# Kernel tuning notes

Measured on AMD Instinct MI355X. Metric: run time of the kernel, lower is better.

## Reference

```python
import jax, jax.numpy as jnp
import numpy as np

D_MODEL = 1024
N_HEADS = 16
HEAD_DIM = D_MODEL // N_HEADS
D_FF = 4096
B, T = 2, 2048


def layernorm(x, g, b, eps=1e-5):
    mu = jnp.mean(x, axis=-1, keepdims=True)
    var = jnp.var(x, axis=-1, keepdims=True)
    return (x - mu) * jax.lax.rsqrt(var + eps) * g + b


def setup_inputs() -> dict:
    key = jax.random.key(0)
    ks = jax.random.split(key, 8)
    s = 0.02
    return {
        "x": jax.random.normal(ks[0], (B, T, D_MODEL), dtype=jnp.float32),
        "ln1_g": jnp.ones((D_MODEL,), jnp.float32),
        "ln1_b": jnp.zeros((D_MODEL,), jnp.float32),
        "qkv_w": jax.random.normal(ks[1], (D_MODEL, 3 * D_MODEL), jnp.float32) * s,
        "qkv_b": jnp.zeros((3 * D_MODEL,), jnp.float32),
        "proj_w": jax.random.normal(ks[2], (D_MODEL, D_MODEL), jnp.float32) * s,
        "proj_b": jnp.zeros((D_MODEL,), jnp.float32),
        "ln2_g": jnp.ones((D_MODEL,), jnp.float32),
        "ln2_b": jnp.zeros((D_MODEL,), jnp.float32),
        "mlp_w1": jax.random.normal(ks[3], (D_MODEL, D_FF), jnp.float32) * s,
        "mlp_b1": jnp.zeros((D_FF,), jnp.float32),
        "mlp_w2": jax.random.normal(ks[4], (D_FF, D_MODEL), jnp.float32) * s,
        "mlp_b2": jnp.zeros((D_MODEL,), jnp.float32),
    }


def reference(x, ln1_g, ln1_b, qkv_w, qkv_b, proj_w, proj_b,
              ln2_g, ln2_b, mlp_w1, mlp_b1, mlp_w2, mlp_b2):
    Bv, Tv, C = x.shape
    scale = HEAD_DIM ** -0.5
    # --- attention branch ---
    h = layernorm(x, ln1_g, ln1_b)
    qkv = h @ qkv_w + qkv_b                                   # [B,T,3C]
    qkv = qkv.reshape(Bv, Tv, 3, N_HEADS, HEAD_DIM)
    q, k, v = qkv[:, :, 0], qkv[:, :, 1], qkv[:, :, 2]        # [B,T,H,Dh]
    att = jnp.einsum('bqhd,bkhd->bhqk', q, k) * scale         # [B,H,T,T]
    causal = jnp.tril(jnp.ones((Tv, Tv), dtype=bool))
    att = jnp.where(causal[None, None], att, -jnp.inf)
    att = jax.nn.softmax(att, axis=-1)
    out = jnp.einsum('bhqk,bkhd->bqhd', att, v).reshape(Bv, Tv, C)
    out = out @ proj_w + proj_b
    x = x + out
    # --- mlp branch ---
    h2 = layernorm(x, ln2_g, ln2_b)
    h2 = jax.nn.gelu(h2 @ mlp_w1 + mlp_b1, approximate=False)
    x = x + (h2 @ mlp_w2 + mlp_b2)
    return x
```

## Files before the change

### kernel.cpp

```cpp
#include <hip/hip_runtime.h>
#include <hip/hip_bf16.h>
#include <cstdint>

typedef __attribute__((ext_vector_type(4))) float f32x4;
typedef __attribute__((ext_vector_type(16))) float f32x16;
typedef __attribute__((ext_vector_type(8))) __bf16 bf16x8;
typedef __attribute__((ext_vector_type(4))) __bf16 bf16x4;
typedef __attribute__((ext_vector_type(4))) uint32_t u32x4;
typedef __attribute__((ext_vector_type(2))) unsigned int u32x2;

#define EPI_BF16  0
#define EPI_GELU  1
#define EPI_RES   2
#define EPI_PART  3
#define EPI_PARTB 4

__device__ __forceinline__ void gll16(const void* g, void* l) {
  __builtin_amdgcn_global_load_lds((__attribute__((address_space(1))) void*)(g),
                                   (__attribute__((address_space(3))) void*)(l), 16, 0, 0);
}

__global__ __launch_bounds__(256)
void convT_all(const float* __restrict__ W0, __bf16* __restrict__ T0,
               const float* __restrict__ W1, __bf16* __restrict__ T1,
               const float* __restrict__ W2, __bf16* __restrict__ T2,
               const float* __restrict__ W3, __bf16* __restrict__ T3)
{
  __shared__ __bf16 t[64][72];
  const int bid = blockIdx.x;
  const float* W; __bf16* WT; int Kd, Nd, nx, lb;
  if (bid < 768)       { W = W0; WT = T0; Kd = 1024; Nd = 3072; nx = 48; lb = bid; }
  else if (bid < 1024) { W = W1; WT = T1; Kd = 1024; Nd = 1024; nx = 16; lb = bid - 768; }
  else if (bid < 2048) { W = W2; WT = T2; Kd = 1024; Nd = 4096; nx = 64; lb = bid - 1024; }
  else                 { W = W3; WT = T3; Kd = 4096; Nd = 1024; nx = 16; lb = bid - 2048; }
  const int tid = threadIdx.x;
  const int n0 = (lb % nx) * 64, k0 = (lb / nx) * 64;
#pragma unroll
  for (int i = 0; i < 4; ++i) {
    const int c = i * 256 + tid;
    const int r = c >> 4, cc = (c & 15) * 4;
    const float4 v = *(const float4*)(W + (size_t)(k0 + r) * Nd + n0 + cc);
    bf16x4 tv; tv[0] = (__bf16)v.x; tv[1] = (__bf16)v.y; tv[2] = (__bf16)v.z; tv[3] = (__bf16)v.w;
    *(bf16x4*)&t[r][cc] = tv;
  }
  __syncthreads();
#pragma unroll
  for (int i = 0; i < 2; ++i) {
    const int c = i * 256 + tid;
    const int n = c >> 3, s = (c & 7) * 8;
    bf16x8 o;
#pragma unroll
    for (int j = 0; j < 8; ++j) o[j] = t[s + j][n];
    *(bf16x8*)(WT + (size_t)(n0 + n) * Kd + k0 + s) = o;
  }
}

__global__ __launch_bounds__(256)
void ln_rows(const float* __restrict__ x, const float* __restrict__ g,
             const float* __restrict__ b, __bf16* __restrict__ out)
{
  const int row = blockIdx.x;
  const int tid = threadIdx.x;
  const float4 v = *(const float4*)(x + (size_t)row * 1024 + tid * 4);
  float s = v.x + v.y + v.z + v.w;
  float q = v.x * v.x + v.y * v.y + v.z * v.z + v.w * v.w;
#pragma unroll
  for (int o = 32; o; o >>= 1) { s += __shfl_xor(s, o); q += __shfl_xor(q, o); }
  __shared__ float red[8];
  const int wid = tid >> 6;
  if ((tid & 63) == 0) { red[wid] = s; red[4 + wid] = q; }
  __syncthreads();
  s = red[0] + red[1] + red[2] + red[3];
  q = red[4] + red[5] + red[6] + red[7];
  const float mu = s * (1.0f / 1024.0f);
  const float var = q * (1.0f / 1024.0f) - mu * mu;
  const float rs = rsqrtf(var + 1e-5f);
  bf16x4 o4;
#pragma unroll
  for (int i = 0; i < 4; ++i) {
    const int c = tid * 4 + i;
    const float xv = (&v.x)[i];
    o4[i] = (__bf16)((xv - mu) * rs * g[c] + b[c]);
  }
  *(bf16x4*)(out + (size_t)row * 1024 + tid * 4) = o4;
}

template<int EPI>
__global__ __launch_bounds__(256)
void gemm_bt(const __bf16* __restrict__ A, const __bf16* __restrict__ BT,
             const float* __restrict__ bias, const float* __restrict__ R,
             void* __restrict__ Out, int M, int N, int K)
{
  const int tid = threadIdx.x;
  const int lane = tid & 63, wid = tid >> 6;
  const int l15 = lane & 15, lg = lane >> 4;
  const int wm = (wid >> 1) * 64, wn = (wid & 1) * 64;
  const int nwg = gridDim.x * gridDim.y;
  const int hw = blockIdx.y * gridDim.x + blockIdx.x;
  const int logical = (hw & 7) * (nwg >> 3) + (hw >> 3);
  const int rowBase = (logical / gridDim.x) * 128;
  const int colBase = (logical % gridDim.x) * 128;
  const int kLen = K / gridDim.z;
  const int kBeg = blockIdx.z * kLen;
  __shared__ __bf16 As[2][128 * 32];
  __shared__ __bf16 Bs[2][128 * 32];
  f32x4 acc[4][4] = {};
  const int fsw = ((l15 >> 1) & 3) << 3;

  auto STAGE = [&](int buf, int k0) {
#pragma unroll
    for (int i = 0; i < 2; ++i) {
      const int c = i * 256 + tid;
      const int r = c >> 2;
      const int s = ((c & 3) ^ ((r >> 1) & 3)) * 8;
      gll16(A + (size_t)(rowBase + r) * K + (k0 + s), &As[buf][c * 8]);
      gll16(BT + (size_t)(colBase + r) * K + (k0 + s), &Bs[buf][c * 8]);
    }
  };

  STAGE(0, kBeg);
  __syncthreads();
  int cur = 0;
  const int kEnd = kBeg + kLen;
  for (int k0 = kBeg; k0 < kEnd; k0 += 32) {
    if (k0 + 32 < kEnd) STAGE(cur ^ 1, k0 + 32);
    bf16x8 af[4], bfr[4];
#pragma unroll
    for (int m = 0; m < 4; ++m) af[m] = *(const bf16x8*)(&As[cur][(wm + m * 16 + l15) * 32 + (lg * 8 ^ fsw)]);
#pragma unroll
    for (int n = 0; n < 4; ++n) bfr[n] = *(const bf16x8*)(&Bs[cur][(wn + n * 16 + l15) * 32 + (lg * 8 ^ fsw)]);
#pragma unroll
    for (int m = 0; m < 4; ++m)
#pragma unroll
      for (int n = 0; n < 4; ++n)
        acc[m][n] = __builtin_amdgcn_mfma_f32_16x16x32_bf16(af[m], bfr[n], acc[m][n], 0, 0, 0);
    __syncthreads();
    cur ^= 1;
  }
#pragma unroll
  for (int m = 0; m < 4; ++m) {
#pragma unroll
    for (int n = 0; n < 4; ++n) {
      const int col = colBase + wn + n * 16 + l15;
      float bb = 0.0f;
      if constexpr (EPI != EPI_PART && EPI != EPI_PARTB) bb = bias[col];
#pragma unroll
      for (int i = 0; i < 4; ++i) {
        const int row = rowBase + wm + m * 16 + lg * 4 + i;
        float v = acc[m][n][i] + bb;
        if constexpr (EPI == EPI_GELU) {
          v = 0.5f * v * (1.0f + erff(v * 0.70710678118654752f));
          ((__bf16*)Out)[(size_t)row * N + col] = (__bf16)v;
        } else if constexpr (EPI == EPI_BF16) {
          ((__bf16*)Out)[(size_t)row * N + col] = (__bf16)v;
        } else if constexpr (EPI == EPI_RES) {
          v += R[(size_t)row * N + col];
          ((float*)Out)[(size_t)row * N + col] = v;
        } else if constexpr (EPI == EPI_PART) {
          ((float*)Out)[((size_t)blockIdx.z * M + row) * N + col] = v;
        } else {
          ((__bf16*)Out)[((size_t)blockIdx.z * M + row) * N + col] = (__bf16)v;
        }
      }
    }
  }
}

__global__ __launch_bounds__(256)
void reduce2(const float* __restrict__ P, const float* __restrict__ bias,
             const float* __restrict__ R, float* __restrict__ Out, int MN, int N)
{
  const size_t e = ((size_t)blockIdx.x * 256 + threadIdx.x) * 4;
  const float4 a = *(const float4*)(P + e);
  const float4 b = *(const float4*)(P + (size_t)MN + e);
  const float4 r = *(const float4*)(R + e);
  const float4 bb = *(const float4*)(bias + (e & (size_t)(N - 1)));
  float4 o;
  o.x = a.x + b.x + r.x + bb.x;
  o.y = a.y + b.y + r.y + bb.y;
  o.z = a.z + b.z + r.z + bb.z;
  o.w = a.w + b.w + r.w + bb.w;
  *(float4*)(Out + e) = o;
}

__global__ __launch_bounds__(256)
void reduce4(const __bf16* __restrict__ P, const float* __restrict__ bias,
             const float* __restrict__ R, float* __restrict__ Out, int MN, int N)
{
  const size_t e = ((size_t)blockIdx.x * 256 + threadIdx.x) * 8;
  float s[8];
#pragma unroll
  for (int i = 0; i < 8; ++i) s[i] = 0.0f;
#pragma unroll
  for (int p = 0; p < 4; ++p) {
    const bf16x8 v = *(const bf16x8*)(P + (size_t)p * MN + e);
#pragma unroll
    for (int i = 0; i < 8; ++i) s[i] += (float)v[i];
  }
  const size_t col = e & (size_t)(N - 1);
  const float4 r0 = *(const float4*)(R + e),       r1 = *(const float4*)(R + e + 4);
  const float4 b0 = *(const float4*)(bias + col),  b1 = *(const float4*)(bias + col + 4);
  float4 o0, o1;
  o0.x = s[0] + r0.x + b0.x; o0.y = s[1] + r0.y + b0.y;
  o0.z = s[2] + r0.z + b0.z; o0.w = s[3] + r0.w + b0.w;
  o1.x = s[4] + r1.x + b1.x; o1.y = s[5] + r1.y + b1.y;
  o1.z = s[6] + r1.z + b1.z; o1.w = s[7] + r1.w + b1.w;
  *(float4*)(Out + e)     = o0;
  *(float4*)(Out + e + 4) = o1;
}

__global__ __launch_bounds__(256)
void rearrange(const __bf16* __restrict__ qkv, __bf16* __restrict__ Q,
               __bf16* __restrict__ Kb, __bf16* __restrict__ VT)
{
  __shared__ __bf16 vt[64][72];
  const int tid = threadIdx.x;
  const int bid = blockIdx.x;
  const int bh = bid >> 5, tt = bid & 31;
  const int b = bh >> 4, h = bh & 15;
  const int t0 = tt * 64;
#pragma unroll
  for (int i = 0; i < 2; ++i) {
    const int c = i * 256 + tid;
    const int tk = c >> 3, d0 = (c & 7) * 8;
    const size_t srow = (size_t)(b * 2048 + t0 + tk) * 3072 + h * 64 + d0;
    const size_t drow = (size_t)(bh * 2048 + t0 + tk) * 64 + d0;
    *(bf16x8*)(Q + drow) = *(const bf16x8*)(qkv + srow);
    *(bf16x8*)(Kb + drow) = *(const bf16x8*)(qkv + srow + 1024);
    *(bf16x8*)&vt[tk][d0] = *(const bf16x8*)(qkv + srow + 2048);
  }
  __syncthreads();
#pragma unroll
  for (int i = 0; i < 2; ++i) {
    const int c = i * 256 + tid;
    const int d = c >> 3, s = (c & 7) * 8;
    bf16x8 o;
#pragma unroll
    for (int j = 0; j < 8; ++j) o[j] = vt[s + j][d];
    *(bf16x8*)(VT + (size_t)(bh * 64 + d) * 2048 + t0 + s) = o;
  }
}

__global__ __launch_bounds__(256)
void attn(const __bf16* __restrict__ Q, const __bf16* __restrict__ K,
          const __bf16* __restrict__ VT, __bf16* __restrict__ O)
{
  const int bid = blockIdx.x;
  const int bh = bid >> 4, qt = 15 - (bid & 15);
  const int tid = threadIdx.x;
  const int lane = tid & 63, w = tid >> 6;
  const int l31 = lane & 31, hi = lane >> 5;
  __shared__ __bf16 Ks[2][64 * 64];
  __shared__ __bf16 Vs[2][64 * 64];
  const size_t base = (size_t)bh * 2048 * 64;
  const int qrow0 = qt * 128 + w * 32;
  const int jd = qrow0 >> 6;
  const int jmax = 2 * qt + 1;
  const int xsw = (l31 & 7) << 3;
  const float KS = 0.18033688011112042f;

  bf16x8 qf[4];
#pragma unroll
  for (int s = 0; s < 4; ++s)
    qf[s] = *(const bf16x8*)(Q + base + (size_t)(qrow0 + l31) * 64 + s * 16 + hi * 8);

  f32x16 oa0 = {}, oa1 = {};
  float ms = -INFINITY, lst = 0.0f;

  auto STAGE = [&](int buf, int j) {
#pragma unroll
    for (int i = 0; i < 2; ++i) {
      const int c = i * 256 + tid;
      const int r = c >> 3;
      const int e = ((c & 7) ^ (r & 7)) * 8;
      gll16(K + base + (size_t)(j * 64 + r) * 64 + e, &Ks[buf][c * 8]);
      gll16(VT + base + (size_t)r * 2048 + j * 64 + e, &Vs[buf][c * 8]);
    }
  };

  STAGE(0, 0);
  __syncthreads();
  int cur = 0;
  for (int j = 0; j <= jmax; ++j) {
    if (j < jmax) STAGE(cur ^ 1, j + 1);
    if (j <= jd) {
      f32x16 s0v = {}, s1v = {};
#pragma unroll
      for (int s = 0; s < 4; ++s) {
        const int co = (s * 16 + hi * 8) ^ xsw;
        bf16x8 ak0 = *(const bf16x8*)(&Ks[cur][l31 * 64 + co]);
        bf16x8 ak1 = *(const bf16x8*)(&Ks[cur][(32 + l31) * 64 + co]);
        s0v = __builtin_amdgcn_mfma_f32_32x32x16_bf16(ak0, qf[s], s0v, 0, 0, 0);
        s1v = __builtin_amdgcn_mfma_f32_32x32x16_bf16(ak1, qf[s], s1v, 0, 0, 0);
      }
      if (j == jd) {
        const int qg = qrow0 + l31;
#pragma unroll
        for (int rg = 0; rg < 16; ++rg) {
          const int kr = j * 64 + ((rg & 3) + 8 * (rg >> 2)) + 4 * hi;
          if (kr > qg) s0v[rg] = -INFINITY;
          if (kr + 32 > qg) s1v[rg] = -INFINITY;
        }
      }
      float mx = fmaxf(s0v[0], s1v[0]);
#pragma unroll
      for (int rg = 1; rg < 16; ++rg) mx = fmaxf(mx, fmaxf(s0v[rg], s1v[rg]));
      mx = fmaxf(mx, __shfl_xor(mx, 32));
      const float mxs = mx * KS;
      if (!__all(mxs - ms <= 8.0f)) {
        const float msn = fmaxf(ms, mxs);
        const float cf = exp2f(ms - msn);
        lst *= cf;
        ms = msn;
#pragma unroll
        for (int rg = 0; rg < 16; ++rg) {
          const float cb = __shfl(cf, (rg & 3) + 8 * (rg >> 2) + 4 * hi);
          oa0[rg] *= cb; oa1[rg] *= cb;
        }
      }
      float rs = 0.0f;
#pragma unroll
      for (int rg = 0; rg < 16; ++rg) {
        const float p0 = exp2f(fmaf(s0v[rg], KS, -ms));
        const float p1 = exp2f(fmaf(s1v[rg], KS, -ms));
        s0v[rg] = p0; s1v[rg] = p1;
        rs += p0 + p1;
      }
      rs += __shfl_xor(rs, 32);
      lst += rs;
#pragma unroll
      for (int s = 0; s < 4; ++s) {
        const int br = (s & 1) * 8;
        uint32_t wA0, wA1, wB0, wB1;
        if (s < 2) {
          asm("v_cvt_pk_bf16_f32 %0, %1, %2" : "=v"(wA0) : "v"(s0v[br + 0]), "v"(s0v[br + 1]));
          asm("v_cvt_pk_bf16_f32 %0, %1, %2" : "=v"(wA1) : "v"(s0v[br + 2]), "v"(s0v[br + 3]));
          asm("v_cvt_pk_bf16_f32 %0, %1, %2" : "=v"(wB0) : "v"(s0v[br + 4]), "v"(s0v[br + 5]));
          asm("v_cvt_pk_bf16_f32 %0, %1, %2" : "=v"(wB1) : "v"(s0v[br + 6]), "v"(s0v[br + 7]));
        } else {
          asm("v_cvt_pk_bf16_f32 %0, %1, %2" : "=v"(wA0) : "v"(s1v[br + 0]), "v"(s1v[br + 1]));
          asm("v_cvt_pk_bf16_f32 %0, %1, %2" : "=v"(wA1) : "v"(s1v[br + 2]), "v"(s1v[br + 3]));
          asm("v_cvt_pk_bf16_f32 %0, %1, %2" : "=v"(wB0) : "v"(s1v[br + 4]), "v"(s1v[br + 5]));
          asm("v_cvt_pk_bf16_f32 %0, %1, %2" : "=v"(wB1) : "v"(s1v[br + 6]), "v"(s1v[br + 7]));
        }
        const u32x2 r0 = __builtin_amdgcn_permlane32_swap(wA0, wB0, false, false);
        const u32x2 r1 = __builtin_amdgcn_permlane32_swap(wA1, wB1, false, false);
        u32x4 uu; uu.x = r0.x; uu.y = r1.x; uu.z = r0.y; uu.w = r1.y;
        const bf16x8 pa = __builtin_bit_cast(bf16x8, uu);
        const int co = (s * 16 + hi * 8) ^ xsw;
        bf16x8 bv0 = *(const bf16x8*)(&Vs[cur][l31 * 64 + co]);
        bf16x8 bv1 = *(const bf16x8*)(&Vs[cur][(32 + l31) * 64 + co]);
        oa0 = __builtin_amdgcn_mfma_f32_32x32x16_bf16(pa, bv0, oa0, 0, 0, 0);
        oa1 = __builtin_amdgcn_mfma_f32_32x32x16_bf16(pa, bv1, oa1, 0, 0, 0);
      }
    }
    __syncthreads();
    cur ^= 1;
  }
  const float inv = 1.0f / lst;
  const int b = bh >> 4, hd = bh & 15;
#pragma unroll
  for (int rg = 0; rg < 16; ++rg) {
    const int cr = (rg & 3) + 8 * (rg >> 2) + 4 * hi;
    const float ib = __shfl(inv, cr);
    const int qr = qrow0 + cr;
    O[(size_t)(b * 2048 + qr) * 1024 + hd * 64 + l31]      = (__bf16)(oa0[rg] * ib);
    O[(size_t)(b * 2048 + qr) * 1024 + hd * 64 + 32 + l31] = (__bf16)(oa1[rg] * ib);
  }
}

extern "C" void kernel_launch(void* const* d_in, const int* in_sizes, int n_in,
                              void* d_out, int out_size, void* d_ws, size_t ws_size,
                              hipStream_t stream)
{
  const float* x      = (const float*)d_in[0];
  const float* ln1_g  = (const float*)d_in[1];
  const float* ln1_b  = (const float*)d_in[2];
  const float* qkv_w  = (const float*)d_in[3];
  const float* qkv_b  = (const float*)d_in[4];
  const float* proj_w = (const float*)d_in[5];
  const float* proj_b = (const float*)d_in[6];
  const float* ln2_g  = (const float*)d_in[7];
  const float* ln2_b  = (const float*)d_in[8];
  const float* mlp_w1 = (const float*)d_in[9];
  const float* mlp_b1 = (const float*)d_in[10];
  const float* mlp_w2 = (const float*)d_in[11];
  const float* mlp_b2 = (const float*)d_in[12];

  char* ws = (char*)d_ws;
  __bf16* qkvT  = (__bf16*)(ws + 0);
  __bf16* projT = (__bf16*)(ws + 6291456);
  __bf16* w1T   = (__bf16*)(ws + 8388608);
  __bf16* w2T   = (__bf16*)(ws + 16777216);
  float*  x2    = (float*) (ws + 25165824);
  __bf16* h1    = (__bf16*)(ws + 41943040);
  float*  partP = (float*) (ws + 41943040);
  __bf16* part2 = (__bf16*)(ws + 41943040);
  __bf16* qkv   = (__bf16*)(ws + 50331648);
  __bf16* Qb    = (__bf16*)(ws + 75497472);
  __bf16* h2    = (__bf16*)(ws + 75497472);
  __bf16* Kb    = (__bf16*)(ws + 83886080);
  __bf16* act1  = (__bf16*)(ws + 83886080);
  __bf16* VTb   = (__bf16*)(ws + 92274688);
  __bf16* attO  = (__bf16*)(ws + 100663296);

  convT_all<<<3072, 256, 0, stream>>>(qkv_w, qkvT, proj_w, projT, mlp_w1, w1T, mlp_w2, w2T);

  ln_rows<<<4096, 256, 0, stream>>>(x, ln1_g, ln1_b, h1);
  gemm_bt<EPI_BF16><<<dim3(24, 32), 256, 0, stream>>>(h1, qkvT, qkv_b, nullptr, qkv, 4096, 3072, 1024);
  rearrange<<<1024, 256, 0, stream>>>(qkv, Qb, Kb, VTb);
  attn<<<512, 256, 0, stream>>>(Qb, Kb, VTb, attO);
  gemm_bt<EPI_PART><<<dim3(8, 32, 2), 256, 0, stream>>>(attO, projT, nullptr, nullptr, partP, 4096, 1024, 1024);
  reduce2<<<4096, 256, 0, stream>>>(partP, proj_b, x, x2, 4096 * 1024, 1024);
  ln_rows<<<4096, 256, 0, stream>>>(x2, ln2_g, ln2_b, h2);
  gemm_bt<EPI_GELU><<<dim3(32, 32), 256, 0, stream>>>(h2, w1T, mlp_b1, nullptr, act1, 4096, 4096, 1024);
  gemm_bt<EPI_PARTB><<<dim3(8, 32, 4), 256, 0, stream>>>(act1, w2T, nullptr, nullptr, part2, 4096, 1024, 4096);
  reduce4<<<2048, 256, 0, stream>>>(part2, mlp_b2, x2, (float*)d_out, 4096 * 1024, 1024);
}
```

Before: 409.3 us.

## Fuse residual reduce with LayerNorm2 and restructure attention to direct-global loads

```diff
diff --git a/kernel.cpp b/kernel.cpp
--- a/kernel.cpp
+++ b/kernel.cpp
@@ -83,6 +83,47 @@
     o4[i] = (__bf16)((xv - mu) * rs * g[c] + b[c]);
   }
   *(bf16x4*)(out + (size_t)row * 1024 + tid * 4) = o4;
+}
+
+__global__ __launch_bounds__(256)
+void reduce2_ln(const float* __restrict__ P, const float* __restrict__ bias,
+                const float* __restrict__ R, const float* __restrict__ g,
+                const float* __restrict__ b, float* __restrict__ x2,
+                __bf16* __restrict__ h2, int MN)
+{
+  const int row = blockIdx.x;
+  const int tid = threadIdx.x;
+  const size_t e = (size_t)row * 1024 + tid * 4;
+  const float4 a  = *(const float4*)(P + e);
+  const float4 p2 = *(const float4*)(P + (size_t)MN + e);
+  const float4 r  = *(const float4*)(R + e);
+  const float4 bi = *(const float4*)(bias + tid * 4);
+  float v[4];
+  v[0] = a.x + p2.x + r.x + bi.x;
+  v[1] = a.y + p2.y + r.y + bi.y;
+  v[2] = a.z + p2.z + r.z + bi.z;
+  v[3] = a.w + p2.w + r.w + bi.w;
+  *(float4*)(x2 + e) = *(float4*)v;
+  float s = v[0] + v[1] + v[2] + v[3];
+  float q = v[0]*v[0] + v[1]*v[1] + v[2]*v[2] + v[3]*v[3];
+#pragma unroll
+  for (int o = 32; o; o >>= 1) { s += __shfl_xor(s, o); q += __shfl_xor(q, o); }
+  __shared__ float red[8];
+  const int wid = tid >> 6;
+  if ((tid & 63) == 0) { red[wid] = s; red[4 + wid] = q; }
+  __syncthreads();
+  s = red[0] + red[1] + red[2] + red[3];
+  q = red[4] + red[5] + red[6] + red[7];
+  const float mu = s * (1.0f / 1024.0f);
+  const float var = q * (1.0f / 1024.0f) - mu * mu;
+  const float rs = rsqrtf(var + 1e-5f);
+  bf16x4 o4;
+#pragma unroll
+  for (int i = 0; i < 4; ++i) {
+    const int c = tid * 4 + i;
+    o4[i] = (__bf16)((v[i] - mu) * rs * g[c] + b[c]);
+  }
+  *(bf16x4*)(h2 + e) = o4;
 }
 
 template<int EPI>
@@ -167,23 +208,6 @@
 }
 
 __global__ __launch_bounds__(256)
-void reduce2(const float* __restrict__ P, const float* __restrict__ bias,
-             const float* __restrict__ R, float* __restrict__ Out, int MN, int N)
-{
-  const size_t e = ((size_t)blockIdx.x * 256 + threadIdx.x) * 4;
-  const float4 a = *(const float4*)(P + e);
-  const float4 b = *(const float4*)(P + (size_t)MN + e);
-  const float4 r = *(const float4*)(R + e);
-  const float4 bb = *(const float4*)(bias + (e & (size_t)(N - 1)));
-  float4 o;
-  o.x = a.x + b.x + r.x + bb.x;
-  o.y = a.y + b.y + r.y + bb.y;
-  o.z = a.z + b.z + r.z + bb.z;
-  o.w = a.w + b.w + r.w + bb.w;
-  *(float4*)(Out + e) = o;
-}
-
-__global__ __launch_bounds__(256)
 void reduce4(const __bf16* __restrict__ P, const float* __restrict__ bias,
              const float* __restrict__ R, float* __restrict__ Out, int MN, int N)
 {
@@ -241,22 +265,17 @@
   }
 }
 
-__global__ __launch_bounds__(256)
+__global__ __launch_bounds__(128)
 void attn(const __bf16* __restrict__ Q, const __bf16* __restrict__ K,
           const __bf16* __restrict__ VT, __bf16* __restrict__ O)
 {
   const int bid = blockIdx.x;
-  const int bh = bid >> 4, qt = 15 - (bid & 15);
+  const int bh = bid >> 5, qt = 31 - (bid & 31);
   const int tid = threadIdx.x;
   const int lane = tid & 63, w = tid >> 6;
   const int l31 = lane & 31, hi = lane >> 5;
-  __shared__ __bf16 Ks[2][64 * 64];
-  __shared__ __bf16 Vs[2][64 * 64];
   const size_t base = (size_t)bh * 2048 * 64;
-  const int qrow0 = qt * 128 + w * 32;
-  const int jd = qrow0 >> 6;
-  const int jmax = 2 * qt + 1;
-  const int xsw = (l31 & 7) << 3;
+  const int qrow0 = qt * 64 + w * 32;
   const float KS = 0.18033688011112042f;
 
   bf16x8 qf[4];
@@ -267,95 +286,81 @@
   f32x16 oa0 = {}, oa1 = {};
   float ms = -INFINITY, lst = 0.0f;
 
-  auto STAGE = [&](int buf, int j) {
-#pragma unroll
-    for (int i = 0; i < 2; ++i) {
-      const int c = i * 256 + tid;
-      const int r = c >> 3;
-      const int e = ((c & 7) ^ (r & 7)) * 8;
-      gll16(K + base + (size_t)(j * 64 + r) * 64 + e, &Ks[buf][c * 8]);
-      gll16(VT + base + (size_t)r * 2048 + j * 64 + e, &Vs[buf][c * 8]);
-    }
-  };
-
-  STAGE(0, 0);
-  __syncthreads();
-  int cur = 0;
-  for (int j = 0; j <= jmax; ++j) {
-    if (j < jmax) STAGE(cur ^ 1, j + 1);
-    if (j <= jd) {
-      f32x16 s0v = {}, s1v = {};
-#pragma unroll
-      for (int s = 0; s < 4; ++s) {
-        const int co = (s * 16 + hi * 8) ^ xsw;
-        bf16x8 ak0 = *(const bf16x8*)(&Ks[cur][l31 * 64 + co]);
-        bf16x8 ak1 = *(const bf16x8*)(&Ks[cur][(32 + l31) * 64 + co]);
-        s0v = __builtin_amdgcn_mfma_f32_32x32x16_bf16(ak0, qf[s], s0v, 0, 0, 0);
-        s1v = __builtin_amdgcn_mfma_f32_32x32x16_bf16(ak1, qf[s], s1v, 0, 0, 0);
+  const __bf16* Krow0 = K + base + (size_t)l31 * 64;
+  const __bf16* Krow1 = K + base + (size_t)(32 + l31) * 64;
+  const __bf16* Vrow0 = VT + base + (size_t)l31 * 2048;
+  const __bf16* Vrow1 = VT + base + (size_t)(32 + l31) * 2048;
+
+  for (int j = 0; j <= qt; ++j) {
+    f32x16 s0v = {}, s1v = {};
+#pragma unroll
+    for (int s = 0; s < 4; ++s) {
+      const int co = s * 16 + hi * 8;
+      bf16x8 ak0 = *(const bf16x8*)(Krow0 + (size_t)j * 4096 + co);
+      bf16x8 ak1 = *(const bf16x8*)(Krow1 + (size_t)j * 4096 + co);
+      s0v = __builtin_amdgcn_mfma_f32_32x32x16_bf16(ak0, qf[s], s0v, 0, 0, 0);
+      s1v = __builtin_amdgcn_mfma_f32_32x32x16_bf16(ak1, qf[s], s1v, 0, 0, 0);
+    }
+    if (j == qt) {
+      const int qg = qrow0 + l31;
+#pragma unroll
+      for (int rg = 0; rg < 16; ++rg) {
+        const int kr = j * 64 + ((rg & 3) + 8 * (rg >> 2)) + 4 * hi;
+        if (kr > qg) s0v[rg] = -INFINITY;
+        if (kr + 32 > qg) s1v[rg] = -INFINITY;
       }
-      if (j == jd) {
-        const int qg = qrow0 + l31;
-#pragma unroll
-        for (int rg = 0; rg < 16; ++rg) {
-          const int kr = j * 64 + ((rg & 3) + 8 * (rg >> 2)) + 4 * hi;
-          if (kr > qg) s0v[rg] = -INFINITY;
-          if (kr + 32 > qg) s1v[rg] = -INFINITY;
-        }
+    }
+    float mx = fmaxf(s0v[0], s1v[0]);
+#pragma unroll
+    for (int rg = 1; rg < 16; ++rg) mx = fmaxf(mx, fmaxf(s0v[rg], s1v[rg]));
+    mx = fmaxf(mx, __shfl_xor(mx, 32));
+    const float mxs = mx * KS;
+    if (!__all(mxs - ms <= 8.0f)) {
+      const float msn = fmaxf(ms, mxs);
+      const float cf = exp2f(ms - msn);
+      lst *= cf;
+      ms = msn;
+#pragma unroll
+      for (int rg = 0; rg < 16; ++rg) {
+        const float cb = __shfl(cf, (rg & 3) + 8 * (rg >> 2) + 4 * hi);
+        oa0[rg] *= cb; oa1[rg] *= cb;
       }
-      float mx = fmaxf(s0v[0], s1v[0]);
-#pragma unroll
-      for (int rg = 1; rg < 16; ++rg) mx = fmaxf(mx, fmaxf(s0v[rg], s1v[rg]));
-      mx = fmaxf(mx, __shfl_xor(mx, 32));
-      const float mxs = mx * KS;
-      if (!__all(mxs - ms <= 8.0f)) {
-        const float msn = fmaxf(ms, mxs);
-        const float cf = exp2f(ms - msn);
-        lst *= cf;
-        ms = msn;
-#pragma unroll
-        for (int rg = 0; rg < 16; ++rg) {
-          const float cb = __shfl(cf, (rg & 3) + 8 * (rg >> 2) + 4 * hi);
-          oa0[rg] *= cb; oa1[rg] *= cb;
-        }
+    }
+    float rs = 0.0f;
+#pragma unroll
+    for (int rg = 0; rg < 16; ++rg) {
+      const float p0 = exp2f(fmaf(s0v[rg], KS, -ms));
+      const float p1 = exp2f(fmaf(s1v[rg], KS, -ms));
+      s0v[rg] = p0; s1v[rg] = p1;
+      rs += p0 + p1;
+    }
+    rs += __shfl_xor(rs, 32);
+    lst += rs;
+#pragma unroll
+    for (int s = 0; s < 4; ++s) {
+      const int br = (s & 1) * 8;
+      uint32_t wA0, wA1, wB0, wB1;
+      if (s < 2) {
+        asm("v_cvt_pk_bf16_f32 %0, %1, %2" : "=v"(wA0) : "v"(s0v[br + 0]), "v"(s0v[br + 1]));
+        asm("v_cvt_pk_bf16_f32 %0, %1, %2" : "=v"(wA1) : "v"(s0v[br + 2]), "v"(s0v[br + 3]));
+        asm("v_cvt_pk_bf16_f32 %0, %1, %2" : "=v"(wB0) : "v"(s0v[br + 4]), "v"(s0v[br + 5]));
+        asm("v_cvt_pk_bf16_f32 %0, %1, %2" : "=v"(wB1) : "v"(s0v[br + 6]), "v"(s0v[br + 7]));
+      } else {
+        asm("v_cvt_pk_bf16_f32 %0, %1, %2" : "=v"(wA0) : "v"(s1v[br + 0]), "v"(s1v[br + 1]));
+        asm("v_cvt_pk_bf16_f32 %0, %1, %2" : "=v"(wA1) : "v"(s1v[br + 2]), "v"(s1v[br + 3]));
+        asm("v_cvt_pk_bf16_f32 %0, %1, %2" : "=v"(wB0) : "v"(s1v[br + 4]), "v"(s1v[br + 5]));
+        asm("v_cvt_pk_bf16_f32 %0, %1, %2" : "=v"(wB1) : "v"(s1v[br + 6]), "v"(s1v[br + 7]));
       }
-      float rs = 0.0f;
-#pragma unroll
-      for (int rg = 0; rg < 16; ++rg) {
-        const float p0 = exp2f(fmaf(s0v[rg], KS, -ms));
-        const float p1 = exp2f(fmaf(s1v[rg], KS, -ms));
-        s0v[rg] = p0; s1v[rg] = p1;
-        rs += p0 + p1;
-      }
-      rs += __shfl_xor(rs, 32);
-      lst += rs;
-#pragma unroll
-      for (int s = 0; s < 4; ++s) {
-        const int br = (s & 1) * 8;
-        uint32_t wA0, wA1, wB0, wB1;
-        if (s < 2) {
-          asm("v_cvt_pk_bf16_f32 %0, %1, %2" : "=v"(wA0) : "v"(s0v[br + 0]), "v"(s0v[br + 1]));
-          asm("v_cvt_pk_bf16_f32 %0, %1, %2" : "=v"(wA1) : "v"(s0v[br + 2]), "v"(s0v[br + 3]));
-          asm("v_cvt_pk_bf16_f32 %0, %1, %2" : "=v"(wB0) : "v"(s0v[br + 4]), "v"(s0v[br + 5]));
-          asm("v_cvt_pk_bf16_f32 %0, %1, %2" : "=v"(wB1) : "v"(s0v[br + 6]), "v"(s0v[br + 7]));
-        } else {
-          asm("v_cvt_pk_bf16_f32 %0, %1, %2" : "=v"(wA0) : "v"(s1v[br + 0]), "v"(s1v[br + 1]));
-          asm("v_cvt_pk_bf16_f32 %0, %1, %2" : "=v"(wA1) : "v"(s1v[br + 2]), "v"(s1v[br + 3]));
-          asm("v_cvt_pk_bf16_f32 %0, %1, %2" : "=v"(wB0) : "v"(s1v[br + 4]), "v"(s1v[br + 5]));
-          asm("v_cvt_pk_bf16_f32 %0, %1, %2" : "=v"(wB1) : "v"(s1v[br + 6]), "v"(s1v[br + 7]));
-        }
-        const u32x2 r0 = __builtin_amdgcn_permlane32_swap(wA0, wB0, false, false);
-        const u32x2 r1 = __builtin_amdgcn_permlane32_swap(wA1, wB1, false, false);
-        u32x4 uu; uu.x = r0.x; uu.y = r1.x; uu.z = r0.y; uu.w = r1.y;
-        const bf16x8 pa = __builtin_bit_cast(bf16x8, uu);
-        const int co = (s * 16 + hi * 8) ^ xsw;
-        bf16x8 bv0 = *(const bf16x8*)(&Vs[cur][l31 * 64 + co]);
-        bf16x8 bv1 = *(const bf16x8*)(&Vs[cur][(32 + l31) * 64 + co]);
-        oa0 = __builtin_amdgcn_mfma_f32_32x32x16_bf16(pa, bv0, oa0, 0, 0, 0);
-        oa1 = __builtin_amdgcn_mfma_f32_32x32x16_bf16(pa, bv1, oa1, 0, 0, 0);
-      }
-    }
-    __syncthreads();
-    cur ^= 1;
+      const u32x2 r0 = __builtin_amdgcn_permlane32_swap(wA0, wB0, false, false);
+      const u32x2 r1 = __builtin_amdgcn_permlane32_swap(wA1, wB1, false, false);
+      u32x4 uu; uu.x = r0.x; uu.y = r1.x; uu.z = r0.y; uu.w = r1.y;
+      const bf16x8 pa = __builtin_bit_cast(bf16x8, uu);
+      const int co = s * 16 + hi * 8;
+      bf16x8 bv0 = *(const bf16x8*)(Vrow0 + (size_t)j * 64 + co);
+      bf16x8 bv1 = *(const bf16x8*)(Vrow1 + (size_t)j * 64 + co);
+      oa0 = __builtin_amdgcn_mfma_f32_32x32x16_bf16(pa, bv0, oa0, 0, 0, 0);
+      oa1 = __builtin_amdgcn_mfma_f32_32x32x16_bf16(pa, bv1, oa1, 0, 0, 0);
+    }
   }
   const float inv = 1.0f / lst;
   const int b = bh >> 4, hd = bh & 15;
@@ -409,10 +414,9 @@
   ln_rows<<<4096, 256, 0, stream>>>(x, ln1_g, ln1_b, h1);
   gemm_bt<EPI_BF16><<<dim3(24, 32), 256, 0, stream>>>(h1, qkvT, qkv_b, nullptr, qkv, 4096, 3072, 1024);
   rearrange<<<1024, 256, 0, stream>>>(qkv, Qb, Kb, VTb);
-  attn<<<512, 256, 0, stream>>>(Qb, Kb, VTb, attO);
+  attn<<<1024, 128, 0, stream>>>(Qb, Kb, VTb, attO);
   gemm_bt<EPI_PART><<<dim3(8, 32, 2), 256, 0, stream>>>(attO, projT, nullptr, nullptr, partP, 4096, 1024, 1024);
-  reduce2<<<4096, 256, 0, stream>>>(partP, proj_b, x, x2, 4096 * 1024, 1024);
-  ln_rows<<<4096, 256, 0, stream>>>(x2, ln2_g, ln2_b, h2);
+  reduce2_ln<<<4096, 256, 0, stream>>>(partP, proj_b, x, ln2_g, ln2_b, x2, h2, 4096 * 1024);
   gemm_bt<EPI_GELU><<<dim3(32, 32), 256, 0, stream>>>(h2, w1T, mlp_b1, nullptr, act1, 4096, 4096, 1024);
   gemm_bt<EPI_PARTB><<<dim3(8, 32, 4), 256, 0, stream>>>(act1, w2T, nullptr, nullptr, part2, 4096, 1024, 4096);
   reduce4<<<2048, 256, 0, stream>>>(part2, mlp_b2, x2, (float*)d_out, 4096 * 1024, 1024);
```

New measurement: 444.2 us. +8.5%, slower.
